# Kernel optimization log

Hardware: AMD Instinct MI355X
Metric: run time of the kernel (lower is better)

Reference implementation:

```python
import jax, jax.numpy as jnp
import numpy as np

B, S, DIM, E, TR, G = 2, 896, 1536, 8, 1643, 8
TYPE_RANGES = ((0, 228), (228, 519), (519, 1286), (1286, 1643))
TOPK = 3


def setup_inputs() -> dict:
    key = jax.random.key(0)
    ks = jax.random.split(key, 16)
    w = 0.02  # weight scale to keep activations sane
    return {
        "x": jax.random.normal(ks[0], (B, S, 2 * DIM), jnp.float32),
        "out": jax.random.normal(ks[1], (B, S, TR), jnp.float32),
        "embedding": jax.random.normal(ks[2], (1, 1, DIM), jnp.float32),
        "index": jax.random.permutation(ks[3], TR).astype(jnp.int32),
        "Wsel": jax.random.normal(ks[4], (2 * DIM, G), jnp.float32) * w,
        "bsel": jax.random.normal(ks[5], (G,), jnp.float32) * w,
        "Wemb": jax.random.normal(ks[6], (DIM, G), jnp.float32) * w,
        "bemb": jax.random.normal(ks[7], (G,), jnp.float32) * w,
        "Wg": jax.random.normal(ks[8], (G, S, E), jnp.float32) * w,
        "bg": jax.random.normal(ks[9], (G, E), jnp.float32) * w,
        "temb": jax.random.normal(ks[10], (4, S), jnp.float32),
        "W1": jax.random.normal(ks[11], (E, S, 2 * S), jnp.float32) * w,
        "b1": jax.random.normal(ks[12], (E, 2 * S), jnp.float32) * w,
        "W2": jax.random.normal(ks[13], (E, 2 * S, S), jnp.float32) * w,
        "b2": jax.random.normal(ks[14], (E, S), jnp.float32) * w,
    }


def reference(x, out, embedding, index, Wsel, bsel, Wemb, bemb, Wg, bg, temb, W1, b1, W2, b2):
    Bb, Ss, Tr = out.shape
    # gate selector inputs: mean-pool x over sequence (AdaptiveAvgPool1d(1))
    gate_logits = x.mean(axis=1) @ Wsel + bsel            # (B, G)
    emb_logits = embedding[:, 0, :] @ Wemb + bemb          # (1, G)
    residual = out
    o = jnp.swapaxes(out, 1, 2)[:, index, :]               # (B, TR, S), gathered track order

    gates_list, weights_list = [], []
    zloss = jnp.zeros((), out.dtype)
    for i, (s0, s1) in enumerate(TYPE_RANGES):
        T = s1 - s0
        temp = (o[:, s0:s1, :] + temb[i]).reshape(Bb * T, Ss)
        tok = gate_logits[:, 2 * i:2 * i + 2]              # (B, 2)
        embl = emb_logits[:, 2 * i:2 * i + 2]              # (1, 2)
        w2 = (jax.nn.softmax(tok, axis=-1) + jax.nn.softmax(embl, axis=-1)) / 2.0  # (B, 2)
        zloss = zloss + jnp.mean(tok ** 2) + jnp.mean(embl ** 2)
        g = jnp.zeros((Bb, T, E), out.dtype)
        for j in range(2):
            logits = jax.nn.leaky_relu(temp @ Wg[2 * i + j] + bg[2 * i + j])  # (B*T, E)
            zloss = zloss + jnp.mean(logits ** 2)
            topv, topi = jax.lax.top_k(logits, TOPK)
            probs = jax.nn.softmax(topv, axis=-1)
            tg = jnp.zeros_like(logits).at[jnp.arange(Bb * T)[:, None], topi].set(probs)
            g = g + tg.reshape(Bb, T, E) * w2[:, j][:, None, None]
        gates_list.append(g)
        weights_list.append(jax.lax.stop_gradient(w2))
    gates = jnp.concatenate(gates_list, axis=1)            # (B, TR, E)
    weights = jnp.concatenate(weights_list, axis=1)        # (B, 8)
    all_gates = jnp.stack([gates[:, s0:s1, :].reshape(-1, E).sum(0) for s0, s1 in TYPE_RANGES])  # (4, E)

    # dense-equivalent of gather -> grouped GEMM -> scatter-add combine
    gf = gates.reshape(Bb * Tr, E)
    xf = o.reshape(Bb * Tr, Ss)
    h = jax.nn.relu(jnp.einsum('ns,esh->neh', xf, W1) + b1[None])  # (N, E, 2S)
    oe = jnp.einsum('neh,ehs->nes', h, W2) + b2[None]              # (N, E, S)
    y = jnp.einsum('ne,nes->ns', gf, oe).reshape(Bb, Tr, Ss)
    yfull = jnp.zeros((Bb, Tr, Ss), out.dtype).at[:, index, :].set(y)
    y_out = jnp.swapaxes(yfull, 1, 2) + residual
    return (y_out, all_gates, zloss, jnp.zeros((), out.dtype), weights)
```

## Files before the change

### kernel.cpp

```cpp
#include <hip/hip_runtime.h>

typedef unsigned short u16;
typedef unsigned int u32;
typedef __bf16 bf16x8 __attribute__((ext_vector_type(8)));
typedef float f32x4 __attribute__((ext_vector_type(4)));
typedef u16 u16x8 __attribute__((ext_vector_type(8)));

#define S_    896
#define TR_   1643
#define NTOK_ 3286
#define MP_   3328

__device__ __forceinline__ u16 f2bf(float f) {
  u32 u = __builtin_bit_cast(u32, f);
  u = (u + 0x7FFFu + ((u >> 16) & 1u)) >> 16;
  return (u16)u;
}

__device__ __forceinline__ void gload16(const void* g, void* l) {
  __builtin_amdgcn_global_load_lds(
      (const __attribute__((address_space(1))) u32*)g,
      (__attribute__((address_space(3))) u32*)l, 16, 0, 0);
}

__global__ void k_init(const int* __restrict__ index, int* __restrict__ inv,
                       float* __restrict__ xmean) {
  int i = blockIdx.x * 256 + threadIdx.x;
  if (i < TR_) inv[index[i]] = i;
  if (i < 6144) xmean[i] = 0.f;
}

__global__ void k_reduce_x(const float* __restrict__ x, float* __restrict__ xmean) {
  int i = blockIdx.x * 256 + threadIdx.x;
  int b = i / 3072, d = i % 3072;
  int s0 = blockIdx.y * 224;
  const float* p = x + (size_t)b * S_ * 3072 + (size_t)s0 * 3072 + d;
  float s = 0.f;
  for (int t = 0; t < 224; ++t) s += p[(size_t)t * 3072];
  atomicAdd(&xmean[i], s * (1.f / (float)S_));
}

__global__ __launch_bounds__(256)
void k_small_dots(const float* __restrict__ xmean,
                  const float* __restrict__ Wsel, const float* __restrict__ bsel,
                  const float* __restrict__ emb,  const float* __restrict__ Wemb,
                  const float* __restrict__ bemb, float* __restrict__ glel) {
  __shared__ float red[256];
  int blk = blockIdx.x, tid = threadIdx.x;
  float s = 0.f;
  if (blk < 16) {
    int b = blk >> 3, g = blk & 7;
    for (int d = tid; d < 3072; d += 256) s += xmean[b * 3072 + d] * Wsel[d * 8 + g];
  } else {
    int g = blk - 16;
    for (int d = tid; d < 1536; d += 256) s += emb[d] * Wemb[d * 8 + g];
  }
  red[tid] = s; __syncthreads();
  for (int st = 128; st > 0; st >>= 1) { if (tid < st) red[tid] += red[tid + st]; __syncthreads(); }
  if (tid == 0) glel[blk] = red[0] + (blk < 16 ? bsel[blk & 7] : bemb[blk - 16]);
}

__global__ void k_small_tail(const float* __restrict__ glel,
                             float* __restrict__ w2buf, float* __restrict__ zpart,
                             float* __restrict__ outw) {
  if (threadIdx.x != 0) return;
  const float* gl = glel;
  const float* el = glel + 16;
  float zp = 0.f;
  for (int i = 0; i < 4; ++i) {
    float e0 = el[2 * i], e1 = el[2 * i + 1];
    float m = fmaxf(e0, e1);
    float x0 = expf(e0 - m), x1 = expf(e1 - m);
    float den = x0 + x1;
    float se0 = x0 / den, se1 = x1 / den;
    zp += (e0 * e0 + e1 * e1) * 0.5f;
    float tsq = 0.f;
    for (int b = 0; b < 2; ++b) {
      float t0 = gl[b * 8 + 2 * i], t1 = gl[b * 8 + 2 * i + 1];
      tsq += t0 * t0 + t1 * t1;
      float mm = fmaxf(t0, t1);
      float y0 = expf(t0 - mm), y1 = expf(t1 - mm);
      float dd = y0 + y1;
      float w0 = (y0 / dd + se0) * 0.5f, w1 = (y1 / dd + se1) * 0.5f;
      w2buf[b * 8 + 2 * i] = w0; w2buf[b * 8 + 2 * i + 1] = w1;
      outw[b * 8 + 2 * i]  = w0; outw[b * 8 + 2 * i + 1]  = w1;
    }
    zp += tsq * 0.25f;
  }
  *zpart = zp;
}

__global__ __launch_bounds__(256)
void k_gather(const float* __restrict__ out_in, const int* __restrict__ inv,
              float* __restrict__ o32) {
  __shared__ float tile[32][33];
  int b = blockIdx.z;
  int tr0 = blockIdx.x * 32, s0 = blockIdx.y * 32;
  int tx = threadIdx.x & 31, ty = threadIdx.x >> 5;
  int ntr = TR_ - tr0; if (ntr > 32) ntr = 32;
  for (int i = ty; i < 32; i += 8)
    tile[i][tx] = (tx < ntr) ? out_in[((size_t)b * S_ + s0 + i) * TR_ + tr0 + tx] : 0.f;
  __syncthreads();
  for (int r = ty; r < ntr; r += 8) {
    int t = inv[tr0 + r];
    o32[((size_t)b * TR_ + t) * S_ + s0 + tx] = tile[tx][r];
  }
}

__global__ __launch_bounds__(256)
void k_gates(const float* __restrict__ o32, const float* __restrict__ temb,
             const float* __restrict__ Wg, const float* __restrict__ bg,
             const float* __restrict__ w2buf, float* __restrict__ gf,
             float* __restrict__ zbuf) {
  int n = blockIdx.x;
  int b = n / TR_, t = n % TR_;
  int typ = (t < 228) ? 0 : (t < 519) ? 1 : (t < 1286) ? 2 : 3;
  int tid = threadIdx.x;
  const float* orow = o32 + (size_t)n * S_;
  const float* trow = temb + typ * S_;
  const float* W0 = Wg + (size_t)(2 * typ) * S_ * 8;

  float acc[16];
#pragma unroll
  for (int k = 0; k < 16; ++k) acc[k] = 0.f;
  for (int s = tid; s < S_; s += 256) {
    float ov = orow[s] + trow[s];
    const float4* wa = (const float4*)(W0 + s * 8);
    const float4* wb = (const float4*)(W0 + 7168 + s * 8);
    float4 a0 = wa[0], a1 = wa[1], b0 = wb[0], b1 = wb[1];
    acc[0]  += ov * a0.x; acc[1]  += ov * a0.y; acc[2]  += ov * a0.z; acc[3]  += ov * a0.w;
    acc[4]  += ov * a1.x; acc[5]  += ov * a1.y; acc[6]  += ov * a1.z; acc[7]  += ov * a1.w;
    acc[8]  += ov * b0.x; acc[9]  += ov * b0.y; acc[10] += ov * b0.z; acc[11] += ov * b0.w;
    acc[12] += ov * b1.x; acc[13] += ov * b1.y; acc[14] += ov * b1.z; acc[15] += ov * b1.w;
  }
#pragma unroll
  for (int k = 0; k < 16; ++k)
#pragma unroll
    for (int m = 1; m < 64; m <<= 1) acc[k] += __shfl_xor(acc[k], m, 64);

  __shared__ float wsum[4][16];
  __shared__ float lgsh[16];
  int w = tid >> 6, lane = tid & 63;
  if (lane == 0)
#pragma unroll
    for (int k = 0; k < 16; ++k) wsum[w][k] = acc[k];
  __syncthreads();
  if (tid < 16)
    lgsh[tid] = wsum[0][tid] + wsum[1][tid] + wsum[2][tid] + wsum[3][tid]
              + bg[(2 * typ + (tid >> 3)) * 8 + (tid & 7)];
  __syncthreads();

  if (tid == 0) {
    float g[8];
    for (int k = 0; k < 8; ++k) g[k] = 0.f;
    float zs[2];
    for (int j = 0; j < 2; ++j) {
      float l[8]; float ss = 0.f;
      for (int k = 0; k < 8; ++k) {
        float v = lgsh[j * 8 + k];
        v = v > 0.f ? v : 0.01f * v;
        l[k] = v; ss += v * v;
      }
      zs[j] = ss;
      int i0 = 0;
      for (int k = 1; k < 8; ++k) if (l[k] > l[i0]) i0 = k;
      int i1 = -1;
      for (int k = 0; k < 8; ++k) { if (k == i0) continue; if (i1 < 0 || l[k] > l[i1]) i1 = k; }
      int i2 = -1;
      for (int k = 0; k < 8; ++k) { if (k == i0 || k == i1) continue; if (i2 < 0 || l[k] > l[i2]) i2 = k; }
      float p1 = expf(l[i1] - l[i0]), p2 = expf(l[i2] - l[i0]);
      float den = 1.f + p1 + p2;
      float w2 = w2buf[b * 8 + 2 * typ + j];
      g[i0] += w2 / den; g[i1] += w2 * p1 / den; g[i2] += w2 * p2 / den;
    }
    float* gfp = gf + (size_t)n * 8;
    for (int k = 0; k < 8; ++k) gfp[k] = g[k];
    zbuf[n * 2 + 0] = zs[0];
    zbuf[n * 2 + 1] = zs[1];
  }
}

__global__ __launch_bounds__(256)
void k_reduce_gates(const float* __restrict__ gf, const float* __restrict__ zbuf,
                    float* __restrict__ allg, float* __restrict__ zsum) {
  __shared__ float red[256];
  const int s0a[4] = {0, 228, 519, 1286};
  const int cta[4] = {228, 291, 767, 357};
  int blk = blockIdx.x, tid = threadIdx.x;
  float s = 0.f;
  if (blk < 32) {
    int typ = blk >> 3, e = blk & 7;
    int s0 = s0a[typ], cnt = cta[typ];
    for (int i = tid; i < 2 * cnt; i += 256) {
      int bb = i / cnt, tt = s0 + i % cnt;
      s += gf[(size_t)(bb * TR_ + tt) * 8 + e];
    }
  } else {
    int idx = blk - 32, typ = idx >> 1, j = idx & 1;
    int s0 = s0a[typ], cnt = cta[typ];
    for (int i = tid; i < 2 * cnt; i += 256) {
      int bb = i / cnt, tt = s0 + i % cnt;
      s += zbuf[(size_t)(bb * TR_ + tt) * 2 + j];
    }
  }
  red[tid] = s; __syncthreads();
  for (int st = 128; st > 0; st >>= 1) { if (tid < st) red[tid] += red[tid + st]; __syncthreads(); }
  if (tid == 0) {
    if (blk < 32) allg[blk] = red[0];
    else          zsum[blk - 32] = red[0];
  }
}

__global__ __launch_bounds__(256)
void k_build_lists(const float* __restrict__ gf, int* __restrict__ listE,
                   float* __restrict__ gcomp, int* __restrict__ posT,
                   int* __restrict__ cntE) {
  __shared__ int wcnt[4];
  __shared__ int sbase;
  int e = blockIdx.x;
  int tid = threadIdx.x, lane = tid & 63, wv = tid >> 6;
  if (tid == 0) sbase = 0;
  __syncthreads();
  for (int c = 0; c < 13; ++c) {
    int n = c * 256 + tid;
    float gv = (n < NTOK_) ? gf[(size_t)n * 8 + e] : 0.f;
    bool flag = (n < NTOK_) && (gv != 0.f);
    unsigned long long m = __ballot(flag);
    if (lane == 0) wcnt[wv] = __popcll(m);
    __syncthreads();
    int prefix = 0;
    for (int w = 0; w < 4; ++w) if (w < wv) prefix += wcnt[w];
    int within = __popcll(m & ((1ull << lane) - 1ull));
    if (n < NTOK_) {
      if (flag) {
        int idx = sbase + prefix + within;
        listE[e * MP_ + idx] = n;
        gcomp[e * MP_ + idx] = gv;
        posT[(size_t)n * 8 + e] = idx;
      } else {
        posT[(size_t)n * 8 + e] = -1;
      }
    }
    __syncthreads();
    if (tid == 0) sbase += wcnt[0] + wcnt[1] + wcnt[2] + wcnt[3];
    __syncthreads();
  }
  if (tid == 0) cntE[e] = sbase;
}

__global__ void k_gatherE(const float* __restrict__ o32, const int* __restrict__ listE,
                          const int* __restrict__ cntE, u16* __restrict__ obfE) {
  int idx = blockIdx.x * 256 + threadIdx.x;
  int g = idx / 112, w8 = (idx % 112) * 8;
  int e = g / MP_, i = g % MP_;
  if (i >= cntE[e]) return;
  int n = listE[g];
  const float* src = o32 + (size_t)n * S_ + w8;
  float4 v0 = *(const float4*)src;
  float4 v1 = *(const float4*)(src + 4);
  u16x8 o;
  o[0] = f2bf(v0.x); o[1] = f2bf(v0.y); o[2] = f2bf(v0.z); o[3] = f2bf(v0.w);
  o[4] = f2bf(v1.x); o[5] = f2bf(v1.y); o[6] = f2bf(v1.z); o[7] = f2bf(v1.w);
  *(u16x8*)(obfE + (size_t)g * S_ + w8) = o;
}

__global__ __launch_bounds__(256)
void k_transpose(const float* __restrict__ W, u16* __restrict__ Wt,
                 int R, int C, int ldo, size_t eo) {
  __shared__ float tile[32][33];
  int e = blockIdx.z;
  const float* Wp = W + (size_t)e * R * C;
  u16* Wtp = Wt + (size_t)e * eo;
  int c0 = blockIdx.x * 32, r0 = blockIdx.y * 32;
  int tx = threadIdx.x & 31, ty = threadIdx.x >> 5;
  for (int i = ty; i < 32; i += 8)
    tile[i][tx] = (c0 + tx < C) ? Wp[(size_t)(r0 + i) * C + c0 + tx] : 0.f;
  __syncthreads();
  for (int i = ty; i < 32; i += 8) Wtp[(size_t)(c0 + i) * ldo + r0 + tx] = f2bf(tile[tx][i]);
}

template <int MODE>
__global__ __launch_bounds__(512, 2)
void k_gemm8s(const u16* __restrict__ A, const u16* __restrict__ Bt,
              const int* __restrict__ cntE,
              const float* __restrict__ gcomp, const float* __restrict__ bias,
              u16* __restrict__ H, u16* __restrict__ Ye) {
  __shared__ __align__(16) u16 lds[2 * 32768];
  const int tid = threadIdx.x;
  const int lane = tid & 63;
  const int wid = tid >> 6;
  const int wr = wid >> 2, wc = wid & 3;

  const int K   = (MODE == 1) ? 896 : 1792;
  const int lda = K, ldb = K;
  const int nx  = (MODE == 1) ? 7 : 4;
  const int n8  = (MODE == 1) ? 91 : 52;
  const size_t bes = (MODE == 1) ? 1605632u : 1835008u;

  int f0 = (blockIdx.z * 13 + blockIdx.y) * nx + blockIdx.x;
  int f = (f0 & 7) * n8 + (f0 >> 3);
  const int ez = f / n8;
  const int r8 = f % n8;
  const int by = r8 / nx, bx = r8 % nx;

  const int cnt = cntE[ez];
  if (by * 256 >= cnt) return;

  const u16* Ag = A + ((size_t)ez * MP_ + (size_t)by * 256) * lda;
  const u16* Bg = Bt + (size_t)ez * bes + (size_t)(bx * 256) * ldb;
  const int NT = K >> 6;

#define SA(buf, g, k0)                                                          \
  { _Pragma("unroll")                                                           \
    for (int q = 0; q < 2; ++q) {                                               \
      const int br = q * 128 + (g) * 64 + wid * 8;                              \
      const int row = br + (lane >> 3);                                         \
      gload16(Ag + (size_t)row * lda + (((lane & 7) ^ (lane >> 3)) << 3) + (k0),\
              lds + (buf) * 32768 + br * 64 + lane * 8);                        \
    } }
#define SB(buf, g, k0)                                                          \
  { _Pragma("unroll")                                                           \
    for (int q = 0; q < 2; ++q) {                                               \
      const int sI = q * 8 + wid;                                               \
      const int br = (sI >> 2) * 64 + (g) * 32 + (sI & 3) * 8;                  \
      const int row = br + (lane >> 3);                                         \
      gload16(Bg + (size_t)row * ldb + (((lane & 7) ^ (lane >> 3)) << 3) + (k0),\
              lds + (buf) * 32768 + 16384 + br * 64 + lane * 8);                \
    } }
#define PSYNC(N)                                             \
  asm volatile("s_waitcnt vmcnt(" #N ")" ::: "memory");      \
  __builtin_amdgcn_s_barrier();                              \
  __builtin_amdgcn_sched_barrier(0);

  const int l15 = lane & 15, l16 = lane >> 4, l7 = lane & 7;
  const int swz0 = (l16 ^ l7) << 3;
  const int swz1 = ((4 + l16) ^ l7) << 3;
  const int rA = (wr * 128 + l15) * 64;
  const int rB = (wc * 64 + l15) * 64;

  f32x4 acc[8][4] = {};
  bf16x8 aF[4][2], b0F[2][2], b1F[2][2];

#define READ_A0  _Pragma("unroll") for (int i = 0; i < 4; ++i) {               \
    aF[i][0] = *(const bf16x8*)(lA + rA + i * 1024 + swz0);                    \
    aF[i][1] = *(const bf16x8*)(lA + rA + i * 1024 + swz1); }
#define READ_A1  _Pragma("unroll") for (int i = 0; i < 4; ++i) {               \
    aF[i][0] = *(const bf16x8*)(lA + rA + (i + 4) * 1024 + swz0);              \
    aF[i][1] = *(const bf16x8*)(lA + rA + (i + 4) * 1024 + swz1); }
#define READ_B0  _Pragma("unroll") for (int j = 0; j < 2; ++j) {               \
    b0F[j][0] = *(const bf16x8*)(lB + rB + j * 1024 + swz0);                   \
    b0F[j][1] = *(const bf16x8*)(lB + rB + j * 1024 + swz1); }
#define READ_B1  _Pragma("unroll") for (int j = 0; j < 2; ++j) {               \
    b1F[j][0] = *(const bf16x8*)(lB + rB + (j + 2) * 1024 + swz0);             \
    b1F[j][1] = *(const bf16x8*)(lB + rB + (j + 2) * 1024 + swz1); }
#define MFMA16(IB, JB, BF)                                                     \
  __builtin_amdgcn_s_setprio(1);                                               \
  _Pragma("unroll") for (int i = 0; i < 4; ++i)                                \
  _Pragma("unroll") for (int j = 0; j < 2; ++j) {                              \
    acc[i + IB][j + JB] = __builtin_amdgcn_mfma_f32_16x16x32_bf16(aF[i][0], BF[j][0], acc[i + IB][j + JB], 0, 0, 0); \
    acc[i + IB][j + JB] = __builtin_amdgcn_mfma_f32_16x16x32_bf16(aF[i][1], BF[j][1], acc[i + IB][j + JB], 0, 0, 0); \
  }                                                                            \
  __builtin_amdgcn_s_setprio(0);

  SA(0, 0, 0) SB(0, 0, 0) SB(0, 1, 0) SA(0, 1, 0)

  int cur = 0;
  for (int t = 0; t < NT - 1; ++t) {
    const u16* lA = lds + cur * 32768;
    const u16* lB = lA + 16384;
    const int nk0 = (t + 1) << 6;
    PSYNC(4)
    SA(cur ^ 1, 0, nk0) SB(cur ^ 1, 0, nk0)
    READ_A0 READ_B0
    MFMA16(0, 0, b0F)
    PSYNC(6)
    SB(cur ^ 1, 1, nk0)
    READ_B1
    MFMA16(0, 2, b1F)
    PSYNC(6)
    SA(cur ^ 1, 1, nk0)
    READ_A1
    MFMA16(4, 2, b1F)
    MFMA16(4, 0, b0F)
    cur ^= 1;
  }
  {
    const u16* lA = lds + cur * 32768;
    const u16* lB = lA + 16384;
    PSYNC(4)
    READ_A0 READ_B0
    MFMA16(0, 0, b0F)
    PSYNC(2)
    READ_B1
    MFMA16(0, 2, b1F)
    PSYNC(0)
    READ_A1
    MFMA16(4, 2, b1F)
    MFMA16(4, 0, b0F)
  }
#undef SA
#undef SB
#undef PSYNC
#undef READ_A0
#undef READ_A1
#undef READ_B0
#undef READ_B1
#undef MFMA16

  if (MODE == 1) {
#pragma unroll
    for (int j = 0; j < 4; ++j) {
      const int col = bx * 256 + wc * 64 + j * 16 + l15;
      const float bia = bias[ez * 1792 + col];
#pragma unroll
      for (int i = 0; i < 8; ++i)
#pragma unroll
        for (int r = 0; r < 4; ++r) {
          const int row = by * 256 + wr * 128 + i * 16 + l16 * 4 + r;
          float v = acc[i][j][r] + bia;
          v = v > 0.f ? v : 0.f;
          H[((size_t)ez * MP_ + row) * 1792 + col] = f2bf(v * gcomp[ez * MP_ + row]);
        }
    }
  } else {
#pragma unroll
    for (int j = 0; j < 4; ++j) {
      const int col = bx * 256 + wc * 64 + j * 16 + l15;
      if (col < 896) {
#pragma unroll
        for (int i = 0; i < 8; ++i)
#pragma unroll
          for (int r = 0; r < 4; ++r) {
            const int row = by * 256 + wr * 128 + i * 16 + l16 * 4 + r;
            Ye[((size_t)ez * MP_ + row) * 896 + col] = f2bf(acc[i][j][r]);
          }
      }
    }
  }
}

__global__ __launch_bounds__(256)
void k_combine(const u16* __restrict__ YeE, const int* __restrict__ posT,
               const float* __restrict__ gf, const float* __restrict__ b2,
               float* __restrict__ yT) {
  __shared__ float tile[32][33];
  int b = blockIdx.z;
  int t0 = blockIdx.x * 32, s0 = blockIdx.y * 32;
  int tx = threadIdx.x & 31, ty = threadIdx.x >> 5;
  int ntv = TR_ - t0; if (ntv > 32) ntv = 32;
  for (int r = ty; r < 32; r += 8) {
    float acc = 0.f;
    if (r < ntv) {
      size_t n = (size_t)b * TR_ + t0 + r;
      const int* pp = posT + n * 8;
      const float* g = gf + n * 8;
      int s = s0 + tx;
#pragma unroll
      for (int e = 0; e < 8; ++e) {
        int p = pp[e];
        if (p >= 0) {
          u32 hv = YeE[((size_t)e * MP_ + p) * 896 + s];
          acc += __builtin_bit_cast(float, hv << 16);
        }
        acc += g[e] * b2[e * 896 + s];
      }
    }
    tile[r][tx] = acc;
  }
  __syncthreads();
  for (int i = ty; i < 32; i += 8)
    if (tx < ntv)
      yT[((size_t)b * S_ + s0 + i) * TR_ + t0 + tx] = tile[tx][i];
}

__global__ void k_scatter(const float* __restrict__ yT, const float* __restrict__ out_in,
                          const int* __restrict__ inv, float* __restrict__ dout,
                          const float* __restrict__ allg, const float* __restrict__ zsum,
                          const float* __restrict__ zpart) {
  int i = blockIdx.x * 256 + threadIdx.x;
  int tr = i % TR_;
  dout[i] = out_in[i] + yT[(size_t)(i - tr) + inv[tr]];
  if (blockIdx.x == 0) {
    int tid = threadIdx.x;
    if (tid < 32) dout[2944256 + tid] = allg[tid];
    else if (tid == 32) {
      float z = *zpart;
      const int Ts[4] = {228, 291, 767, 357};
      for (int q = 0; q < 4; ++q)
        for (int j = 0; j < 2; ++j)
          z += zsum[q * 2 + j] / (float)(2 * Ts[q] * 8);
      dout[2944288] = z;
      dout[2944289] = 0.f;
    }
  }
}

extern "C" void kernel_launch(void* const* d_in, const int* in_sizes, int n_in,
                              void* d_out, int out_size, void* d_ws, size_t ws_size,
                              hipStream_t stream) {
  const float* x         = (const float*)d_in[0];
  const float* out_in    = (const float*)d_in[1];
  const float* embedding = (const float*)d_in[2];
  const int*   index     = (const int*)d_in[3];
  const float* Wsel      = (const float*)d_in[4];
  const float* bsel      = (const float*)d_in[5];
  const float* Wemb      = (const float*)d_in[6];
  const float* bemb      = (const float*)d_in[7];
  const float* Wg        = (const float*)d_in[8];
  const float* bg        = (const float*)d_in[9];
  const float* temb      = (const float*)d_in[10];
  const float* W1        = (const float*)d_in[11];
  const float* b1        = (const float*)d_in[12];
  const float* W2        = (const float*)d_in[13];
  const float* b2        = (const float*)d_in[14];
  float* dout = (float*)d_out;

  char* ws = (char*)d_ws;
  float* allg  = (float*)(ws + 0);
  float* zsum  = (float*)(ws + 128);
  float* zpart = (float*)(ws + 160);
  float* w2buf = (float*)(ws + 192);
  int*   inv   = (int*)(ws + 256);
  float* glel  = (float*)(ws + 6912);
  int*   cntE  = (int*)(ws + 7040);
  float* xmean = (float*)(ws + 8192);
  float* gf    = (float*)(ws + 32768);
  float* o32   = (float*)(ws + 139264);
  float* yT    = o32;
  float* zbuf  = (float*)(ws + 139264 + (size_t)NTOK_ * S_ * 4);
  int*   posT  = (int*)(ws + 12066816);
  int*   listE = (int*)(ws + 12171968);
  float* gcomp = (float*)(ws + 12278464);
  u16*   w1t   = (u16*)(ws + 12386304);
  u16*   w2tE  = (u16*)(ws + 38076416);
  u16*   obfE  = (u16*)(ws + 67436544);
  u16*   YeE   = obfE;
  u16*   HbE   = (u16*)(ws + 115146752);

  k_init<<<26, 256, 0, stream>>>(index, inv, xmean);
  k_reduce_x<<<dim3(24, 4), 256, 0, stream>>>(x, xmean);
  k_small_dots<<<24, 256, 0, stream>>>(xmean, Wsel, bsel, embedding, Wemb, bemb, glel);
  k_small_tail<<<1, 64, 0, stream>>>(glel, w2buf, zpart, dout + 2944290);
  k_gather<<<dim3(52, 28, 2), 256, 0, stream>>>(out_in, inv, o32);
  k_gates<<<NTOK_, 256, 0, stream>>>(o32, temb, Wg, bg, w2buf, gf, zbuf);
  k_reduce_gates<<<40, 256, 0, stream>>>(gf, zbuf, allg, zsum);

  k_build_lists<<<8, 256, 0, stream>>>(gf, listE, gcomp, posT, cntE);
  k_gatherE<<<11648, 256, 0, stream>>>(o32, listE, cntE, obfE);

  k_transpose<<<dim3(56, 28, 8), 256, 0, stream>>>(W1, w1t, 896, 1792, 896, (size_t)1605632);
  k_gemm8s<1><<<dim3(7, 13, 8), 512, 0, stream>>>(obfE, w1t, cntE, gcomp, b1, HbE, nullptr);

  k_transpose<<<dim3(32, 56, 8), 256, 0, stream>>>(W2, w2tE, 1792, 896, 1792, (size_t)1835008);
  k_gemm8s<2><<<dim3(4, 13, 8), 512, 0, stream>>>(HbE, w2tE, cntE, nullptr, nullptr, nullptr, YeE);

  k_combine<<<dim3(52, 28, 2), 256, 0, stream>>>(YeE, posT, gf, b2, yT);
  k_scatter<<<11501, 256, 0, stream>>>(yT, out_in, inv, dout, allg, zsum, zpart);
}
```

Baseline: 389.5 us.

## Fuse expert row gather into first GEMM A-loads and drop gatherE kernel

The first expert GEMM now loads A rows indirectly through the per-expert token list, reading a bf16 copy of the gathered activations that k_gather writes alongside the fp32 copy. This removes the k_gatherE kernel and its materialized per-expert bf16 buffer. The list tail is zero-padded so padded rows read a valid row. The x mean-reduction also drops its split-plus-atomics scheme for one full-length loop per thread, which removes the zero-init but launches far fewer blocks.

```diff
diff --git a/kernel.cpp b/kernel.cpp
--- a/kernel.cpp
+++ b/kernel.cpp
@@ -23,21 +23,19 @@
       (__attribute__((address_space(3))) u32*)l, 16, 0, 0);
 }
 
-__global__ void k_init(const int* __restrict__ index, int* __restrict__ inv,
-                       float* __restrict__ xmean) {
+__global__ void k_init(const int* __restrict__ index, int* __restrict__ inv) {
   int i = blockIdx.x * 256 + threadIdx.x;
   if (i < TR_) inv[index[i]] = i;
-  if (i < 6144) xmean[i] = 0.f;
-}
-
-__global__ void k_reduce_x(const float* __restrict__ x, float* __restrict__ xmean) {
+}
+
+__global__ __launch_bounds__(256)
+void k_reduce_x(const float* __restrict__ x, float* __restrict__ xmean) {
   int i = blockIdx.x * 256 + threadIdx.x;
   int b = i / 3072, d = i % 3072;
-  int s0 = blockIdx.y * 224;
-  const float* p = x + (size_t)b * S_ * 3072 + (size_t)s0 * 3072 + d;
+  const float* p = x + (size_t)b * S_ * 3072 + d;
   float s = 0.f;
-  for (int t = 0; t < 224; ++t) s += p[(size_t)t * 3072];
-  atomicAdd(&xmean[i], s * (1.f / (float)S_));
+  for (int t = 0; t < S_; ++t) s += p[(size_t)t * 3072];
+  xmean[i] = s * (1.f / (float)S_);
 }
 
 __global__ __launch_bounds__(256)
@@ -92,7 +90,7 @@
 
 __global__ __launch_bounds__(256)
 void k_gather(const float* __restrict__ out_in, const int* __restrict__ inv,
-              float* __restrict__ o32) {
+              float* __restrict__ o32, u16* __restrict__ obf) {
   __shared__ float tile[32][33];
   int b = blockIdx.z;
   int tr0 = blockIdx.x * 32, s0 = blockIdx.y * 32;
@@ -103,7 +101,10 @@
   __syncthreads();
   for (int r = ty; r < ntr; r += 8) {
     int t = inv[tr0 + r];
-    o32[((size_t)b * TR_ + t) * S_ + s0 + tx] = tile[tx][r];
+    size_t off = ((size_t)b * TR_ + t) * S_ + s0 + tx;
+    float v = tile[tx][r];
+    o32[off] = v;
+    obf[off] = f2bf(v);
   }
 }
 
@@ -245,23 +246,11 @@
     if (tid == 0) sbase += wcnt[0] + wcnt[1] + wcnt[2] + wcnt[3];
     __syncthreads();
   }
+  for (int idx = sbase + tid; idx < MP_; idx += 256) {
+    listE[e * MP_ + idx] = 0;
+    gcomp[e * MP_ + idx] = 0.f;
+  }
   if (tid == 0) cntE[e] = sbase;
-}
-
-__global__ void k_gatherE(const float* __restrict__ o32, const int* __restrict__ listE,
-                          const int* __restrict__ cntE, u16* __restrict__ obfE) {
-  int idx = blockIdx.x * 256 + threadIdx.x;
-  int g = idx / 112, w8 = (idx % 112) * 8;
-  int e = g / MP_, i = g % MP_;
-  if (i >= cntE[e]) return;
-  int n = listE[g];
-  const float* src = o32 + (size_t)n * S_ + w8;
-  float4 v0 = *(const float4*)src;
-  float4 v1 = *(const float4*)(src + 4);
-  u16x8 o;
-  o[0] = f2bf(v0.x); o[1] = f2bf(v0.y); o[2] = f2bf(v0.z); o[3] = f2bf(v0.w);
-  o[4] = f2bf(v1.x); o[5] = f2bf(v1.y); o[6] = f2bf(v1.z); o[7] = f2bf(v1.w);
-  *(u16x8*)(obfE + (size_t)g * S_ + w8) = o;
 }
 
 __global__ __launch_bounds__(256)
@@ -282,7 +271,7 @@
 template <int MODE>
 __global__ __launch_bounds__(512, 2)
 void k_gemm8s(const u16* __restrict__ A, const u16* __restrict__ Bt,
-              const int* __restrict__ cntE,
+              const int* __restrict__ listE, const int* __restrict__ cntE,
               const float* __restrict__ gcomp, const float* __restrict__ bias,
               u16* __restrict__ H, u16* __restrict__ Ye) {
   __shared__ __align__(16) u16 lds[2 * 32768];
@@ -306,25 +295,40 @@
   const int cnt = cntE[ez];
   if (by * 256 >= cnt) return;
 
-  const u16* Ag = A + ((size_t)ez * MP_ + (size_t)by * 256) * lda;
+  const int scol = ((lane & 7) ^ (lane >> 3)) << 3;
+  const int rl   = wid * 8 + (lane >> 3);
+
+  const u16* aB00; const u16* aB01; const u16* aB10; const u16* aB11;
+  if (MODE == 1) {
+    const int* lE = listE + ez * MP_ + by * 256;
+    aB00 = A + (size_t)lE[rl]       * 896 + scol;
+    aB10 = A + (size_t)lE[64 + rl]  * 896 + scol;
+    aB01 = A + (size_t)lE[128 + rl] * 896 + scol;
+    aB11 = A + (size_t)lE[192 + rl] * 896 + scol;
+  } else {
+    const u16* Ag = A + ((size_t)ez * MP_ + (size_t)by * 256) * lda;
+    aB00 = Ag + (size_t)rl * lda + scol;
+    aB10 = Ag + (size_t)(64 + rl) * lda + scol;
+    aB01 = Ag + (size_t)(128 + rl) * lda + scol;
+    aB11 = Ag + (size_t)(192 + rl) * lda + scol;
+  }
   const u16* Bg = Bt + (size_t)ez * bes + (size_t)(bx * 256) * ldb;
   const int NT = K >> 6;
 
 #define SA(buf, g, k0)                                                          \
-  { _Pragma("unroll")                                                           \
-    for (int q = 0; q < 2; ++q) {                                               \
-      const int br = q * 128 + (g) * 64 + wid * 8;                              \
-      const int row = br + (lane >> 3);                                         \
-      gload16(Ag + (size_t)row * lda + (((lane & 7) ^ (lane >> 3)) << 3) + (k0),\
-              lds + (buf) * 32768 + br * 64 + lane * 8);                        \
-    } }
+  {                                                                             \
+    gload16((g ? aB10 : aB00) + (k0),                                           \
+            lds + (buf) * 32768 + ((g) * 64 + wid * 8) * 64 + lane * 8);        \
+    gload16((g ? aB11 : aB01) + (k0),                                           \
+            lds + (buf) * 32768 + (128 + (g) * 64 + wid * 8) * 64 + lane * 8);  \
+  }
 #define SB(buf, g, k0)                                                          \
   { _Pragma("unroll")                                                           \
     for (int q = 0; q < 2; ++q) {                                               \
       const int sI = q * 8 + wid;                                               \
       const int br = (sI >> 2) * 64 + (g) * 32 + (sI & 3) * 8;                  \
       const int row = br + (lane >> 3);                                         \
-      gload16(Bg + (size_t)row * ldb + (((lane & 7) ^ (lane >> 3)) << 3) + (k0),\
+      gload16(Bg + (size_t)row * ldb + scol + (k0),                             \
               lds + (buf) * 32768 + 16384 + br * 64 + lane * 8);                \
     } }
 #define PSYNC(N)                                             \
@@ -528,31 +532,29 @@
   float* o32   = (float*)(ws + 139264);
   float* yT    = o32;
   float* zbuf  = (float*)(ws + 139264 + (size_t)NTOK_ * S_ * 4);
-  int*   posT  = (int*)(ws + 12066816);
-  int*   listE = (int*)(ws + 12171968);
-  float* gcomp = (float*)(ws + 12278464);
-  u16*   w1t   = (u16*)(ws + 12386304);
-  u16*   w2tE  = (u16*)(ws + 38076416);
-  u16*   obfE  = (u16*)(ws + 67436544);
-  u16*   YeE   = obfE;
-  u16*   HbE   = (u16*)(ws + 115146752);
-
-  k_init<<<26, 256, 0, stream>>>(index, inv, xmean);
-  k_reduce_x<<<dim3(24, 4), 256, 0, stream>>>(x, xmean);
+  u16*   obf   = (u16*)(ws + 12066816);
+  int*   posT  = (int*)(ws + 18030592);
+  int*   listE = (int*)(ws + 18135744);
+  float* gcomp = (float*)(ws + 18242240);
+  u16*   w1t   = (u16*)(ws + 18350080);
+  u16*   w2tE  = (u16*)(ws + 44040192);
+  u16*   HbE   = (u16*)(ws + 73400320);
+  u16*   YeE   = (u16*)(ws + 168820736);
+
+  k_init<<<7, 256, 0, stream>>>(index, inv);
+  k_reduce_x<<<24, 256, 0, stream>>>(x, xmean);
   k_small_dots<<<24, 256, 0, stream>>>(xmean, Wsel, bsel, embedding, Wemb, bemb, glel);
   k_small_tail<<<1, 64, 0, stream>>>(glel, w2buf, zpart, dout + 2944290);
-  k_gather<<<dim3(52, 28, 2), 256, 0, stream>>>(out_in, inv, o32);
+  k_gather<<<dim3(52, 28, 2), 256, 0, stream>>>(out_in, inv, o32, obf);
   k_gates<<<NTOK_, 256, 0, stream>>>(o32, temb, Wg, bg, w2buf, gf, zbuf);
   k_reduce_gates<<<40, 256, 0, stream>>>(gf, zbuf, allg, zsum);
-
   k_build_lists<<<8, 256, 0, stream>>>(gf, listE, gcomp, posT, cntE);
-  k_gatherE<<<11648, 256, 0, stream>>>(o32, listE, cntE, obfE);
 
   k_transpose<<<dim3(56, 28, 8), 256, 0, stream>>>(W1, w1t, 896, 1792, 896, (size_t)1605632);
-  k_gemm8s<1><<<dim3(7, 13, 8), 512, 0, stream>>>(obfE, w1t, cntE, gcomp, b1, HbE, nullptr);
+  k_gemm8s<1><<<dim3(7, 13, 8), 512, 0, stream>>>(obf, w1t, listE, cntE, gcomp, b1, HbE, nullptr);
 
   k_transpose<<<dim3(32, 56, 8), 256, 0, stream>>>(W2, w2tE, 1792, 896, 1792, (size_t)1835008);
-  k_gemm8s<2><<<dim3(4, 13, 8), 512, 0, stream>>>(HbE, w2tE, cntE, nullptr, nullptr, nullptr, YeE);
+  k_gemm8s<2><<<dim3(4, 13, 8), 512, 0, stream>>>(HbE, w2tE, listE, cntE, nullptr, nullptr, nullptr, YeE);
 
   k_combine<<<dim3(52, 28, 2), 256, 0, stream>>>(YeE, posT, gf, b2, yT);
   k_scatter<<<11501, 256, 0, stream>>>(yT, out_in, inv, dout, allg, zsum, zpart);
```

Measured after the change: 418.0 us. 7.3% more time.
